# Performance work log

Measured on AMD Instinct MI355X. Metric: run time of the kernel, lower is better.

The kernel has to match this reference:

```python
import jax, jax.numpy as jnp
import numpy as np

N, NOBJ, M, H, W = 512, 16, 8192, 128, 128


def _rand_rotations(key, n):
    A = jax.random.normal(key, (n, 3, 3), dtype=jnp.float32)
    q, r = jnp.linalg.qr(A)
    q = q * jnp.sign(jnp.diagonal(r, axis1=-2, axis2=-1))[:, None, :]
    det = jnp.linalg.det(q)  # +-1; flip first column if det == -1
    q = q.at[:, :, 0].multiply(det[:, None])
    return q


def setup_inputs() -> dict:
    key = jax.random.key(0)
    ks = jax.random.split(key, 10)
    obj_id = jax.random.randint(ks[0], (N,), 0, NOBJ, dtype=jnp.int32)
    # realistic pinhole intrinsics (pixels), slight per-sample jitter
    base_K = jnp.array([[600.0, 0.0, 64.0], [0.0, 600.0, 64.0], [0.0, 0.0, 1.0]], jnp.float32)
    cam_K = base_K[None] + jax.random.normal(ks[1], (N, 3, 3)) * jnp.array(
        [[5.0, 0.0, 1.0], [0.0, 5.0, 1.0], [0.0, 0.0, 0.0]], jnp.float32)
    gt_R = _rand_rotations(ks[2], N)
    # small rotational perturbation for pred
    pred_R = _rand_rotations(ks[3], N) @ gt_R
    gt_t = jnp.concatenate([jax.random.normal(ks[4], (N, 2)) * 20.0,
                            500.0 + jax.random.uniform(ks[4], (N, 1)) * 300.0], axis=-1)
    pred_t = gt_t + jax.random.normal(ks[5], (N, 3)) * 5.0
    mesh_points = jax.random.normal(ks[6], (NOBJ, M, 3)) * 50.0  # mm-scale meshes
    diameters = 150.0 + jax.random.uniform(ks[7], (NOBJ,)) * 150.0
    gt_coord_3d_roi = jax.random.normal(ks[8], (N, 3, H, W)) * 50.0
    gt_mask_vis_roi = jax.random.bernoulli(ks[9], 0.4, (N, 1, H, W))
    return dict(obj_id=obj_id, cam_K=cam_K, gt_cam_R_m2c=gt_R, gt_cam_t_m2c=gt_t,
                pred_cam_R_m2c=pred_R, pred_cam_t_m2c=pred_t,
                gt_coord_3d_roi=gt_coord_3d_roi, gt_mask_vis_roi=gt_mask_vis_roi,
                mesh_points=mesh_points, diameters=diameters)


def _project(K, x):
    # K: [N,3,3], x: [N,...,3] -> pixel coords [N,...,2]
    h = jnp.einsum('nij,n...j->n...i', K, x)
    return h[..., :2] / h[..., 2:3]


def reference(obj_id, cam_K, gt_cam_R_m2c, gt_cam_t_m2c, pred_cam_R_m2c,
              pred_cam_t_m2c, gt_coord_3d_roi, gt_mask_vis_roi, mesh_points, diameters):
    # RE (degrees)
    R_diff = pred_cam_R_m2c @ jnp.swapaxes(gt_cam_R_m2c, -2, -1)
    trace = R_diff[..., 0, 0] + R_diff[..., 1, 1] + R_diff[..., 2, 2]
    re = jnp.arccos((jnp.clip(trace, -1.0, 3.0) - 1.0) * 0.5) * (180.0 / jnp.pi)
    # TE (cm)
    te = jnp.linalg.norm(pred_cam_t_m2c - gt_cam_t_m2c, axis=-1) * 100.0
    # ADD: mean distance between transformed mesh points, / diameter
    pts = mesh_points[obj_id]                      # [N,M,3]
    dR = pred_cam_R_m2c - gt_cam_R_m2c
    dt = pred_cam_t_m2c - gt_cam_t_m2c
    diff = jnp.einsum('nij,nmj->nmi', dR, pts) + dt[:, None, :]
    ad = jnp.linalg.norm(diff, axis=-1).mean(axis=-1) / diameters[obj_id]
    # PROJ: mean projected distance over mesh points
    xp = jnp.einsum('nij,nmj->nmi', pred_cam_R_m2c, pts) + pred_cam_t_m2c[:, None, :]
    xg = jnp.einsum('nij,nmj->nmi', gt_cam_R_m2c, pts) + gt_cam_t_m2c[:, None, :]
    pj = jnp.linalg.norm(_project(cam_K, xp) - _project(cam_K, xg), axis=-1).mean(axis=-1)
    # PROJ-visible: same over visible ROI pixels (masked mean instead of ragged gather)
    verts = jnp.transpose(gt_coord_3d_roi, (0, 2, 3, 1))  # [N,H,W,3]
    vp = jnp.einsum('nij,nhwj->nhwi', pred_cam_R_m2c, verts) + pred_cam_t_m2c[:, None, None, :]
    vg = jnp.einsum('nij,nhwj->nhwi', gt_cam_R_m2c, verts) + gt_cam_t_m2c[:, None, None, :]
    d = jnp.linalg.norm(_project(cam_K, vp) - _project(cam_K, vg), axis=-1)  # [N,H,W]
    mask = gt_mask_vis_roi[:, 0].astype(d.dtype)
    pv = (d * mask).sum(axis=(1, 2)) / jnp.maximum(mask.sum(axis=(1, 2)), 1.0)
    return re, te, ad, pj, pv
```

## Files before the change

### kernel.cpp

```cpp
#include <hip/hip_runtime.h>
#include <math.h>

#define NS   512
#define NOBJ 16
#define MPTS 8192
#define HH   128
#define WW   128
#define HW   (HH * WW)
#define BLOCK 1024
#define NWAVE (BLOCK / 64)

__device__ __forceinline__ void project(const float K[9], float x, float y, float z,
                                        float& u, float& v) {
    float w  = K[6] * x + K[7] * y + K[8] * z;
    float iw = 1.0f / w;
    u = (K[0] * x + K[1] * y + K[2] * z) * iw;
    v = (K[3] * x + K[4] * y + K[5] * z) * iw;
}

__global__ __launch_bounds__(BLOCK) void score_kernel(
    const int*   __restrict__ obj_id,
    const float* __restrict__ cam_K,
    const float* __restrict__ gt_R,
    const float* __restrict__ gt_t,
    const float* __restrict__ pr_R,
    const float* __restrict__ pr_t,
    const float* __restrict__ coord,
    const int*   __restrict__ mask,
    const float* __restrict__ mesh,
    const float* __restrict__ diam,
    float*       __restrict__ out)
{
    const int n   = blockIdx.x;
    const int tid = threadIdx.x;

    float K[9], Rg[9], Rp[9];
    float tg[3], tp[3];
#pragma unroll
    for (int i = 0; i < 9; ++i) {
        K[i]  = cam_K[n * 9 + i];
        Rg[i] = gt_R [n * 9 + i];
        Rp[i] = pr_R [n * 9 + i];
    }
#pragma unroll
    for (int i = 0; i < 3; ++i) {
        tg[i] = gt_t[n * 3 + i];
        tp[i] = pr_t[n * 3 + i];
    }
    const int   obj = obj_id[n];
    const float dia = diam[obj];

    float dR[9], dt[3];
#pragma unroll
    for (int i = 0; i < 9; ++i) dR[i] = Rp[i] - Rg[i];
#pragma unroll
    for (int i = 0; i < 3; ++i) dt[i] = tp[i] - tg[i];

    float s_ad = 0.0f, s_pj = 0.0f;
    const float* mp = mesh + (size_t)obj * MPTS * 3;
#pragma unroll
    for (int it = 0; it < MPTS / BLOCK; ++it) {
        const int m = it * BLOCK + tid;
        const float px = mp[m * 3 + 0];
        const float py = mp[m * 3 + 1];
        const float pz = mp[m * 3 + 2];
        const float dx = dR[0] * px + dR[1] * py + dR[2] * pz + dt[0];
        const float dy = dR[3] * px + dR[4] * py + dR[5] * pz + dt[1];
        const float dz = dR[6] * px + dR[7] * py + dR[8] * pz + dt[2];
        s_ad += sqrtf(dx * dx + dy * dy + dz * dz);
        const float apx = Rp[0] * px + Rp[1] * py + Rp[2] * pz + tp[0];
        const float apy = Rp[3] * px + Rp[4] * py + Rp[5] * pz + tp[1];
        const float apz = Rp[6] * px + Rp[7] * py + Rp[8] * pz + tp[2];
        const float agx = Rg[0] * px + Rg[1] * py + Rg[2] * pz + tg[0];
        const float agy = Rg[3] * px + Rg[4] * py + Rg[5] * pz + tg[1];
        const float agz = Rg[6] * px + Rg[7] * py + Rg[8] * pz + tg[2];
        float up, vp, ug, vg;
        project(K, apx, apy, apz, up, vp);
        project(K, agx, agy, agz, ug, vg);
        const float du = up - ug, dv = vp - vg;
        s_pj += sqrtf(du * du + dv * dv);
    }

    const float* cx = coord + (size_t)n * 3 * HW;
    const float* cy = cx + HW;
    const float* cz = cy + HW;
    const int*   mk = mask + (size_t)n * HW;

    float s_pv = 0.0f, s_m = 0.0f;
    const float4* cx4 = (const float4*)cx;
    const float4* cy4 = (const float4*)cy;
    const float4* cz4 = (const float4*)cz;
    const int4*   mk4 = (const int4*)mk;

#pragma unroll
    for (int it = 0; it < HW / 4 / BLOCK; ++it) {
        const int p = it * BLOCK + tid;
        const float4 vx = cx4[p];
        const float4 vy = cy4[p];
        const float4 vz = cz4[p];
        const int4   mm = mk4[p];

        const float xs[4] = {vx.x, vx.y, vx.z, vx.w};
        const float ys[4] = {vy.x, vy.y, vy.z, vy.w};
        const float zs[4] = {vz.x, vz.y, vz.z, vz.w};
        const int   ms[4] = {mm.x, mm.y, mm.z, mm.w};

#pragma unroll
        for (int j = 0; j < 4; ++j) {
            const float x = xs[j], y = ys[j], z = zs[j];
            const float apx = Rp[0] * x + Rp[1] * y + Rp[2] * z + tp[0];
            const float apy = Rp[3] * x + Rp[4] * y + Rp[5] * z + tp[1];
            const float apz = Rp[6] * x + Rp[7] * y + Rp[8] * z + tp[2];
            const float agx = Rg[0] * x + Rg[1] * y + Rg[2] * z + tg[0];
            const float agy = Rg[3] * x + Rg[4] * y + Rg[5] * z + tg[1];
            const float agz = Rg[6] * x + Rg[7] * y + Rg[8] * z + tg[2];
            float up, vp, ug, vg;
            project(K, apx, apy, apz, up, vp);
            project(K, agx, agy, agz, ug, vg);
            const float du = up - ug, dv = vp - vg;
            const float d  = sqrtf(du * du + dv * dv);
            const float fm = (ms[j] != 0) ? 1.0f : 0.0f;
            s_pv += d * fm;
            s_m  += fm;
        }
    }

    float vals[4] = {s_ad, s_pj, s_pv, s_m};
#pragma unroll
    for (int k = 0; k < 4; ++k) {
#pragma unroll
        for (int off = 32; off > 0; off >>= 1)
            vals[k] += __shfl_down(vals[k], off, 64);
    }

    __shared__ float red[4][NWAVE];
    const int wave = tid >> 6;
    const int lane = tid & 63;
    if (lane == 0) {
#pragma unroll
        for (int k = 0; k < 4; ++k) red[k][wave] = vals[k];
    }
    __syncthreads();

    if (tid == 0) {
        float tot[4];
#pragma unroll
        for (int k = 0; k < 4; ++k) {
            float s = 0.0f;
#pragma unroll
            for (int w = 0; w < NWAVE; ++w) s += red[k][w];
            tot[k] = s;
        }

        float trace = 0.0f;
#pragma unroll
        for (int i = 0; i < 9; ++i) trace += Rp[i] * Rg[i];
        trace = fminf(fmaxf(trace, -1.0f), 3.0f);
        const float re = acosf((trace - 1.0f) * 0.5f) * (180.0f / 3.14159265358979323846f);

        const float te = sqrtf(dt[0] * dt[0] + dt[1] * dt[1] + dt[2] * dt[2]) * 100.0f;

        out[0 * NS + n] = re;
        out[1 * NS + n] = te;
        out[2 * NS + n] = tot[0] * (1.0f / MPTS) / dia;
        out[3 * NS + n] = tot[1] * (1.0f / MPTS);
        out[4 * NS + n] = tot[2] / fmaxf(tot[3], 1.0f);
    }
}

extern "C" void kernel_launch(void* const* d_in, const int* in_sizes, int n_in,
                              void* d_out, int out_size, void* d_ws, size_t ws_size,
                              hipStream_t stream) {
    const int*   obj_id = (const int*)  d_in[0];
    const float* cam_K  = (const float*)d_in[1];
    const float* gt_R   = (const float*)d_in[2];
    const float* gt_t   = (const float*)d_in[3];
    const float* pr_R   = (const float*)d_in[4];
    const float* pr_t   = (const float*)d_in[5];
    const float* coord  = (const float*)d_in[6];
    const int*   mask   = (const int*)  d_in[7];
    const float* mesh   = (const float*)d_in[8];
    const float* diam   = (const float*)d_in[9];
    float* out = (float*)d_out;

    score_kernel<<<NS, BLOCK, 0, stream>>>(obj_id, cam_K, gt_R, gt_t, pr_R, pr_t,
                                           coord, mask, mesh, diam, out);
}
```

Before: 192.4 us.

## Fold intrinsics into rotations, use fast rcp/sqrt, vectorize mesh loads

Precomputes K·R and K·t per sample so each point needs one affine map per pose instead of a rotation followed by a projection. Replaces IEEE division and sqrtf with AMDGCN native rcp/sqrt intrinsics. Loads mesh points as three float4 per four points instead of scalar strided loads. This cuts ALU work and the cost of the accurate divide sequence, at the price of slightly lower precision from the approximate reciprocal and sqrt.

After: 190.5 us. Within noise of the previous version (-1.0%).

```diff
diff --git a/kernel.cpp b/kernel.cpp
--- a/kernel.cpp
+++ b/kernel.cpp
@@ -10,13 +10,8 @@
 #define BLOCK 1024
 #define NWAVE (BLOCK / 64)
 
-__device__ __forceinline__ void project(const float K[9], float x, float y, float z,
-                                        float& u, float& v) {
-    float w  = K[6] * x + K[7] * y + K[8] * z;
-    float iw = 1.0f / w;
-    u = (K[0] * x + K[1] * y + K[2] * z) * iw;
-    v = (K[3] * x + K[4] * y + K[5] * z) * iw;
-}
+__device__ __forceinline__ float frcp(float x)  { return __builtin_amdgcn_rcpf(x); }
+__device__ __forceinline__ float fsqrt(float x) { return __builtin_amdgcn_sqrtf(x); }
 
 __global__ __launch_bounds__(BLOCK) void score_kernel(
     const int*   __restrict__ obj_id,
@@ -34,8 +29,7 @@
     const int n   = blockIdx.x;
     const int tid = threadIdx.x;
 
-    float K[9], Rg[9], Rp[9];
-    float tg[3], tp[3];
+    float K[9], Rg[9], Rp[9], tg[3], tp[3];
 #pragma unroll
     for (int i = 0; i < 9; ++i) {
         K[i]  = cam_K[n * 9 + i];
@@ -56,42 +50,62 @@
 #pragma unroll
     for (int i = 0; i < 3; ++i) dt[i] = tp[i] - tg[i];
 
+    float Ap[9], Ag[9], bp[3], bg[3];
+#pragma unroll
+    for (int r = 0; r < 3; ++r) {
+#pragma unroll
+        for (int c = 0; c < 3; ++c) {
+            Ap[r * 3 + c] = K[r * 3 + 0] * Rp[0 * 3 + c]
+                          + K[r * 3 + 1] * Rp[1 * 3 + c]
+                          + K[r * 3 + 2] * Rp[2 * 3 + c];
+            Ag[r * 3 + c] = K[r * 3 + 0] * Rg[0 * 3 + c]
+                          + K[r * 3 + 1] * Rg[1 * 3 + c]
+                          + K[r * 3 + 2] * Rg[2 * 3 + c];
+        }
+        bp[r] = K[r * 3 + 0] * tp[0] + K[r * 3 + 1] * tp[1] + K[r * 3 + 2] * tp[2];
+        bg[r] = K[r * 3 + 0] * tg[0] + K[r * 3 + 1] * tg[1] + K[r * 3 + 2] * tg[2];
+    }
+
     float s_ad = 0.0f, s_pj = 0.0f;
-    const float* mp = mesh + (size_t)obj * MPTS * 3;
-#pragma unroll
-    for (int it = 0; it < MPTS / BLOCK; ++it) {
-        const int m = it * BLOCK + tid;
-        const float px = mp[m * 3 + 0];
-        const float py = mp[m * 3 + 1];
-        const float pz = mp[m * 3 + 2];
-        const float dx = dR[0] * px + dR[1] * py + dR[2] * pz + dt[0];
-        const float dy = dR[3] * px + dR[4] * py + dR[5] * pz + dt[1];
-        const float dz = dR[6] * px + dR[7] * py + dR[8] * pz + dt[2];
-        s_ad += sqrtf(dx * dx + dy * dy + dz * dz);
-        const float apx = Rp[0] * px + Rp[1] * py + Rp[2] * pz + tp[0];
-        const float apy = Rp[3] * px + Rp[4] * py + Rp[5] * pz + tp[1];
-        const float apz = Rp[6] * px + Rp[7] * py + Rp[8] * pz + tp[2];
-        const float agx = Rg[0] * px + Rg[1] * py + Rg[2] * pz + tg[0];
-        const float agy = Rg[3] * px + Rg[4] * py + Rg[5] * pz + tg[1];
-        const float agz = Rg[6] * px + Rg[7] * py + Rg[8] * pz + tg[2];
-        float up, vp, ug, vg;
-        project(K, apx, apy, apz, up, vp);
-        project(K, agx, agy, agz, ug, vg);
-        const float du = up - ug, dv = vp - vg;
-        s_pj += sqrtf(du * du + dv * dv);
+
+    const float4* mp4 = (const float4*)(mesh + (size_t)obj * MPTS * 3);
+#pragma unroll
+    for (int it = 0; it < MPTS / (BLOCK * 4); ++it) {
+        const int k = it * BLOCK + tid;
+        const float4 f0 = mp4[k * 3 + 0];
+        const float4 f1 = mp4[k * 3 + 1];
+        const float4 f2 = mp4[k * 3 + 2];
+        const float px[4] = {f0.x, f0.w, f1.z, f2.y};
+        const float py[4] = {f0.y, f1.x, f1.w, f2.z};
+        const float pz[4] = {f0.z, f1.y, f2.x, f2.w};
+#pragma unroll
+        for (int j = 0; j < 4; ++j) {
+            const float x = px[j], y = py[j], z = pz[j];
+            const float dx = fmaf(dR[0], x, fmaf(dR[1], y, fmaf(dR[2], z, dt[0])));
+            const float dy = fmaf(dR[3], x, fmaf(dR[4], y, fmaf(dR[5], z, dt[1])));
+            const float dz = fmaf(dR[6], x, fmaf(dR[7], y, fmaf(dR[8], z, dt[2])));
+            s_ad += fsqrt(fmaf(dx, dx, fmaf(dy, dy, dz * dz)));
+            const float hpx = fmaf(Ap[0], x, fmaf(Ap[1], y, fmaf(Ap[2], z, bp[0])));
+            const float hpy = fmaf(Ap[3], x, fmaf(Ap[4], y, fmaf(Ap[5], z, bp[1])));
+            const float hpz = fmaf(Ap[6], x, fmaf(Ap[7], y, fmaf(Ap[8], z, bp[2])));
+            const float hgx = fmaf(Ag[0], x, fmaf(Ag[1], y, fmaf(Ag[2], z, bg[0])));
+            const float hgy = fmaf(Ag[3], x, fmaf(Ag[4], y, fmaf(Ag[5], z, bg[1])));
+            const float hgz = fmaf(Ag[6], x, fmaf(Ag[7], y, fmaf(Ag[8], z, bg[2])));
+            const float iwp = frcp(hpz), iwg = frcp(hgz);
+            const float du = fmaf(hpx, iwp, -hgx * iwg);
+            const float dv = fmaf(hpy, iwp, -hgy * iwg);
+            s_pj += fsqrt(fmaf(du, du, dv * dv));
+        }
     }
 
     const float* cx = coord + (size_t)n * 3 * HW;
-    const float* cy = cx + HW;
-    const float* cz = cy + HW;
     const int*   mk = mask + (size_t)n * HW;
+    const float4* cx4 = (const float4*)cx;
+    const float4* cy4 = (const float4*)(cx + HW);
+    const float4* cz4 = (const float4*)(cx + 2 * HW);
+    const int4*   mk4 = (const int4*)mk;
 
     float s_pv = 0.0f, s_m = 0.0f;
-    const float4* cx4 = (const float4*)cx;
-    const float4* cy4 = (const float4*)cy;
-    const float4* cz4 = (const float4*)cz;
-    const int4*   mk4 = (const int4*)mk;
-
 #pragma unroll
     for (int it = 0; it < HW / 4 / BLOCK; ++it) {
         const int p = it * BLOCK + tid;
@@ -108,17 +122,16 @@
 #pragma unroll
         for (int j = 0; j < 4; ++j) {
             const float x = xs[j], y = ys[j], z = zs[j];
-            const float apx = Rp[0] * x + Rp[1] * y + Rp[2] * z + tp[0];
-            const float apy = Rp[3] * x + Rp[4] * y + Rp[5] * z + tp[1];
-            const float apz = Rp[6] * x + Rp[7] * y + Rp[8] * z + tp[2];
-            const float agx = Rg[0] * x + Rg[1] * y + Rg[2] * z + tg[0];
-            const float agy = Rg[3] * x + Rg[4] * y + Rg[5] * z + tg[1];
-            const float agz = Rg[6] * x + Rg[7] * y + Rg[8] * z + tg[2];
-            float up, vp, ug, vg;
-            project(K, apx, apy, apz, up, vp);
-            project(K, agx, agy, agz, ug, vg);
-            const float du = up - ug, dv = vp - vg;
-            const float d  = sqrtf(du * du + dv * dv);
+            const float hpx = fmaf(Ap[0], x, fmaf(Ap[1], y, fmaf(Ap[2], z, bp[0])));
+            const float hpy = fmaf(Ap[3], x, fmaf(Ap[4], y, fmaf(Ap[5], z, bp[1])));
+            const float hpz = fmaf(Ap[6], x, fmaf(Ap[7], y, fmaf(Ap[8], z, bp[2])));
+            const float hgx = fmaf(Ag[0], x, fmaf(Ag[1], y, fmaf(Ag[2], z, bg[0])));
+            const float hgy = fmaf(Ag[3], x, fmaf(Ag[4], y, fmaf(Ag[5], z, bg[1])));
+            const float hgz = fmaf(Ag[6], x, fmaf(Ag[7], y, fmaf(Ag[8], z, bg[2])));
+            const float iwp = frcp(hpz), iwg = frcp(hgz);
+            const float du = fmaf(hpx, iwp, -hgx * iwg);
+            const float dv = fmaf(hpy, iwp, -hgy * iwg);
+            const float d  = fsqrt(fmaf(du, du, dv * dv));
             const float fm = (ms[j] != 0) ? 1.0f : 0.0f;
             s_pv += d * fm;
             s_m  += fm;
@@ -157,7 +170,6 @@
         for (int i = 0; i < 9; ++i) trace += Rp[i] * Rg[i];
         trace = fminf(fmaxf(trace, -1.0f), 3.0f);
         const float re = acosf((trace - 1.0f) * 0.5f) * (180.0f / 3.14159265358979323846f);
-
         const float te = sqrtf(dt[0] * dt[0] + dt[1] * dt[1] + dt[2] * dt[2]) * 100.0f;
 
         out[0 * NS + n] = re;
```
